# Kernel optimization log

Hardware: AMD Instinct MI355X
Metric: run time of the kernel (lower is better)

Reference implementation:

```python
import jax, jax.numpy as jnp
import numpy as np

N = 100000   # nodes
E = 1600000  # edges (avg degree 16)
G = 1024     # graphs in batch
F = 128      # node feature dim
H = 128      # hidden channels


def setup_inputs() -> dict:
    key = jax.random.key(0)
    ks = jax.random.split(key, 12)
    s = 1.0 / np.sqrt(H)
    x = jax.random.normal(ks[0], (N, F), dtype=jnp.float32)
    edge_index = jax.random.randint(ks[1], (2, E), 0, N, dtype=jnp.int32)
    batch = jnp.sort(jax.random.randint(ks[2], (N,), 0, G, dtype=jnp.int32))
    return {
        "x": x,
        "edge_index": edge_index,
        "batch": batch,
        "W1": jax.random.normal(ks[3], (F, H), dtype=jnp.float32) * s,
        "b1": jnp.zeros((H,), jnp.float32),
        "W2": jax.random.normal(ks[4], (H, H), dtype=jnp.float32) * s,
        "b2": jnp.zeros((H,), jnp.float32),
        "W3": jax.random.normal(ks[5], (H, H), dtype=jnp.float32) * s,
        "b3": jnp.zeros((H,), jnp.float32),
        "W4": jax.random.normal(ks[6], (H, H), dtype=jnp.float32) * s,
        "b4": jnp.zeros((H,), jnp.float32),
        "linW": jax.random.normal(ks[7], (H, 2), dtype=jnp.float32) * s,
        "linb": jnp.zeros((2,), jnp.float32),
    }


def _gcn_conv(h, W, b, src, dst, norm, n):
    # h' = D^{-1/2}(A+I)D^{-1/2} (h W) + b   (PyG GCNConv default)
    m = h @ W                              # [n, H]
    msg = m[src] * norm[:, None]           # [E+n, H] gather + scale
    out = jax.ops.segment_sum(msg, dst, num_segments=n)
    return out + b


def reference(x, edge_index, batch, W1, b1, W2, b2, W3, b3, W4, b4, linW, linb):
    n = x.shape[0]
    loops = jnp.arange(n, dtype=edge_index.dtype)
    src = jnp.concatenate([edge_index[0], loops])   # add self-loops
    dst = jnp.concatenate([edge_index[1], loops])
    deg = jax.ops.segment_sum(jnp.ones_like(dst, dtype=x.dtype), dst, num_segments=n)
    dinv = jax.lax.rsqrt(deg)                       # deg >= 1 due to self-loops
    norm = dinv[src] * dinv[dst]                    # [E+n]

    h = jax.nn.relu(_gcn_conv(x, W1, b1, src, dst, norm, n))
    h = jax.nn.relu(_gcn_conv(h, W2, b2, src, dst, norm, n))
    h = jax.nn.relu(_gcn_conv(h, W3, b3, src, dst, norm, n))
    h = jax.nn.relu(_gcn_conv(h, W4, b4, src, dst, norm, n))

    # global_mean_pool over `batch` segment ids
    counts = jax.ops.segment_sum(jnp.ones((n,), x.dtype), batch, num_segments=G)
    pooled = jax.ops.segment_sum(h, batch, num_segments=G) / jnp.maximum(counts, 1.0)[:, None]

    # dropout p=0.5 is identity in eval mode
    return pooled @ linW + linb
```

## Files before the change

### kernel.cpp

```cpp
#include <hip/hip_runtime.h>
#include <math.h>

#define NF 128
#define NU 64
#define NQ 32
#define TROWS 32
#define ARS 68
#define CRS 132
#define QS  16.0f
#define QIS 0.0625f

#define SRC_BITS 18
#define SRC_MASK ((1u << SRC_BITS) - 1u)
#define BCS 32
#define EPB 2048

typedef unsigned int  u32;
typedef unsigned short u16;
typedef u32 b4 __attribute__((ext_vector_type(2)));
typedef short bf16x8 __attribute__((ext_vector_type(8)));
typedef float f32x4 __attribute__((ext_vector_type(4)));
typedef float f32x2 __attribute__((ext_vector_type(2)));

__device__ inline u16 f2bf(float f) {
    u32 u = __float_as_uint(f);
    return (u16)((u + 0x7fffu + ((u >> 16) & 1u)) >> 16);
}
__device__ inline u32 pack2(float a, float b) {
    return (u32)f2bf(a) | ((u32)f2bf(b) << 16);
}
__device__ inline float bflo(u32 u) { return __uint_as_float(u << 16); }
__device__ inline float bfhi(u32 u) { return __uint_as_float(u & 0xffff0000u); }

__device__ inline u32 pack4(float a, float b, float c, float d) {
    u32 v = __builtin_amdgcn_cvt_pk_fp8_f32(a, b, 0, false);
    v = __builtin_amdgcn_cvt_pk_fp8_f32(c, d, v, true);
    return v;
}
__device__ inline void acc4(float4& a, u32 q) {
    f32x2 lo = __builtin_amdgcn_cvt_pk_f32_fp8(q, false);
    f32x2 hi = __builtin_amdgcn_cvt_pk_f32_fp8(q, true);
    a.x += lo[0]; a.y += lo[1]; a.z += hi[0]; a.w += hi[1];
}


__global__ __launch_bounds__(256) void k_bcnt(const int* __restrict__ ei,
                                              int* bcnt, int E, int bshift) {
    __shared__ int h[256];
    int t = threadIdx.x;
    h[t] = 0;
    __syncthreads();
    int base = blockIdx.x * EPB;
    #pragma unroll
    for (int k = 0; k < EPB / 256; ++k) {
        int e = base + k * 256 + t;
        if (e < E) atomicAdd(&h[ei[E + e] >> bshift], 1);
    }
    __syncthreads();
    if (h[t]) atomicAdd(&bcnt[t * BCS], h[t]);
}

__global__ __launch_bounds__(256) void k_bscan(const int* __restrict__ bcnt,
                                               int* bbase, int* bcur) {
    __shared__ int s[256];
    int t = threadIdx.x;
    int v = bcnt[t * BCS];
    s[t] = v;
    for (int d = 1; d < 256; d <<= 1) {
        __syncthreads();
        int a = (t >= d) ? s[t - d] : 0;
        __syncthreads();
        s[t] += a;
    }
    __syncthreads();
    bbase[t + 1] = s[t];
    bcur[t * BCS] = s[t] - v;
    if (t == 0) bbase[0] = 0;
}

__global__ __launch_bounds__(256) void k_bscat(const int* __restrict__ ei,
                                               int* bcur, u32* __restrict__ pairs,
                                               int E, int bshift) {
    __shared__ int h[256];
    __shared__ int rb[256];
    int t = threadIdx.x;
    h[t] = 0;
    __syncthreads();
    int base = blockIdx.x * EPB;
    #pragma unroll
    for (int k = 0; k < EPB / 256; ++k) {
        int e = base + k * 256 + t;
        if (e < E) atomicAdd(&h[ei[E + e] >> bshift], 1);
    }
    __syncthreads();
    int c = h[t];
    if (c) rb[t] = atomicAdd(&bcur[t * BCS], c);
    h[t] = 0;
    __syncthreads();
    #pragma unroll
    for (int k = 0; k < EPB / 256; ++k) {
        int e = base + k * 256 + t;
        if (e < E) {
            int d = ei[E + e];
            int b = d >> bshift;
            int p = rb[b] + atomicAdd(&h[b], 1);
            u32 rel = (u32)(d - (b << bshift));
            pairs[p] = (rel << SRC_BITS) | (u32)ei[e];
        }
    }
}

__global__ __launch_bounds__(512) void k_degscan(const u32* __restrict__ pairs,
        const int* __restrict__ bbase, float* __restrict__ dinv,
        int* __restrict__ offs, int* __restrict__ bsum, int n, int bshift) {
    extern __shared__ int sh[];
    int bsz = 1 << bshift;
    int* deg = sh;
    int* ss = sh + bsz;
    int b = blockIdx.x, b0 = b << bshift, t = threadIdx.x;
    for (int i = t; i < bsz; i += 512) deg[i] = 0;
    __syncthreads();
    int lo = bbase[b], hi = bbase[b + 1];
    for (int j = lo + t; j < hi; j += 512)
        atomicAdd(&deg[pairs[j] >> SRC_BITS], 1);
    __syncthreads();
    int C = bsz >> 9;
    int vloc[8];
    int tsum = 0;
    for (int c = 0; c < C; ++c) {
        int i = t * C + c;
        int node = b0 + i;
        int v = 0;
        if (node < n) {
            int real = deg[i] + 1;
            dinv[node] = 1.0f / sqrtf((float)real);
            v = (real + 3) & ~3;
        }
        vloc[c] = tsum;
        tsum += v;
    }
    ss[t] = tsum;
    for (int d = 1; d < 512; d <<= 1) {
        __syncthreads();
        int a = (t >= d) ? ss[t - d] : 0;
        __syncthreads();
        ss[t] += a;
    }
    __syncthreads();
    int tbase = ss[t] - tsum;
    for (int c = 0; c < C; ++c) {
        int node = b0 + t * C + c;
        if (node < n) offs[node] = tbase + vloc[c];
    }
    if (t == 511) bsum[b] = ss[511];
}

__global__ __launch_bounds__(256) void k_bktscan(int* bsum, int* offs,
                                                 int nbk, int n) {
    __shared__ int s[256];
    int t = threadIdx.x;
    int v = (t < nbk) ? bsum[t] : 0;
    s[t] = v;
    for (int d = 1; d < 256; d <<= 1) {
        __syncthreads();
        int a = (t >= d) ? s[t - d] : 0;
        __syncthreads();
        s[t] += a;
    }
    __syncthreads();
    if (t < nbk) bsum[t] = s[t] - v;
    if (t == 255) offs[n] = s[255];
}

__global__ __launch_bounds__(512) void k_csr(const u32* __restrict__ pairs,
        const int* __restrict__ bbase, const int* __restrict__ bsum,
        int* __restrict__ offs, int* __restrict__ srcS,
        int n, int nbk, int bshift) {
    extern __shared__ int sh[];
    int bsz = 1 << bshift;
    int* cur = sh;
    int* endv = sh + bsz;
    int b = blockIdx.x, b0 = b << bshift, t = threadIdx.x;
    int base = bsum[b];
    for (int i = t; i < bsz; i += 512) {
        int node = b0 + i;
        int o = 0;
        if (node < n) {
            o = offs[node] + base;
            offs[node] = o;
        }
        cur[i] = o;
    }
    __syncthreads();
    int offs_n = offs[n];
    for (int i = t; i < bsz; i += 512) {
        int node = b0 + i;
        int e;
        if (i < bsz - 1) e = (node + 1 < n) ? cur[i + 1] : offs_n;
        else             e = (b + 1 < nbk) ? bsum[b + 1] : offs_n;
        endv[i] = e;
    }
    __syncthreads();
    int lo = bbase[b], hi = bbase[b + 1];
    for (int j = lo + t; j < hi; j += 512) {
        u32 v = pairs[j];
        int p = atomicAdd(&cur[v >> SRC_BITS], 1);
        srcS[p] = (int)(v & SRC_MASK);
    }
    __syncthreads();
    for (int i = t; i < bsz; i += 512) {
        int node = b0 + i;
        if (node < n) {
            int c = cur[i];
            srcS[c] = node;
            int e = endv[i];
            for (int k = c + 1; k < e; ++k) srcS[k] = n;
        }
    }
}

__global__ __launch_bounds__(256) void k_pack(const float* __restrict__ x,
                       const float* __restrict__ dinv, u32* __restrict__ q,
                       const float* __restrict__ W0, const float* __restrict__ W1,
                       const float* __restrict__ W2, const float* __restrict__ W3,
                       u32* __restrict__ wt, int n) {
    int t = blockIdx.x * blockDim.x + threadIdx.x;
    int totalu4 = (n + 1) * (NQ / 4);
    if (t < totalu4) {
        int row = t >> 3;
        uint4 o = make_uint4(0, 0, 0, 0);
        if (row < n) {
            int cbase = (t & 7) << 4;
            const float* xr = x + (size_t)row * NF + cbase;
            float4 f0 = *(const float4*)(xr);
            float4 f1 = *(const float4*)(xr + 4);
            float4 f2 = *(const float4*)(xr + 8);
            float4 f3 = *(const float4*)(xr + 12);
            float d = dinv[row] * QS;
            o.x = pack4(f0.x * d, f0.y * d, f0.z * d, f0.w * d);
            o.y = pack4(f1.x * d, f1.y * d, f1.z * d, f1.w * d);
            o.z = pack4(f2.x * d, f2.y * d, f2.z * d, f2.w * d);
            o.w = pack4(f3.x * d, f3.y * d, f3.z * d, f3.w * d);
        }
        ((uint4*)q)[t] = o;
    }
    if (t < 4 * 2048) {
        int layer = t >> 11;
        int rem = t & 2047;
        int lane = rem & 63;
        int ks = (rem >> 6) & 3;
        int nt = rem >> 8;
        const float* W = layer == 0 ? W0 : layer == 1 ? W1 : layer == 2 ? W2 : W3;
        int nn = nt * 16 + (lane & 15);
        int k0 = ks * 32 + (lane >> 4) * 8;
        uint4 o;
        o.x = pack2(W[(k0 + 0) * NF + nn], W[(k0 + 1) * NF + nn]);
        o.y = pack2(W[(k0 + 2) * NF + nn], W[(k0 + 3) * NF + nn]);
        o.z = pack2(W[(k0 + 4) * NF + nn], W[(k0 + 5) * NF + nn]);
        o.w = pack2(W[(k0 + 6) * NF + nn], W[(k0 + 7) * NF + nn]);
        ((uint4*)wt)[t] = o;
    }
}

__global__ __launch_bounds__(256, 8) void k_fused(
        const u32* __restrict__ hin, const int* __restrict__ offs,
        const int* __restrict__ srcS, const float* __restrict__ dinv,
        const u32* __restrict__ wt, const float* __restrict__ bias,
        u32* __restrict__ out, int* tctr, int n, int ntiles, int last) {
    __shared__ __align__(16) u32 buf[TROWS * CRS];
    __shared__ int stile;
    float* Cs = (float*)buf;
    int tid = threadIdx.x;
    int grp = tid >> 5;
    int lane32 = tid & 31;
    int c4 = lane32 << 2;
    int cu = lane32 << 1;
    int cq = lane32;
    int wv = tid >> 6;
    int lane = tid & 63;
    int m0 = (wv & 1) * 16;
    int nh = wv >> 1;
    int mrow = lane & 15, quad = lane >> 4;

    float4 bv = *(const float4*)(bias + c4);

    for (;;) {
        if (tid == 0) stile = atomicAdd(tctr, 1);
        __syncthreads();
        int tile = stile;
        if (tile >= ntiles) break;
        int row0 = tile * TROWS;

        #pragma unroll
        for (int i = 0; i < 4; ++i) {
            int r = grp * 4 + i;
            int node = row0 + r;
            float4 acc = make_float4(0.f, 0.f, 0.f, 0.f);
            if (node < n) {
                int b = offs[node], e = offs[node + 1];
                int j = b;
                for (; j + 8 <= e; j += 8) {
                    int4 sa = *(const int4*)(srcS + j);
                    int4 sb = *(const int4*)(srcS + j + 4);
                    u32 q0 = hin[(size_t)sa.x * NQ + cq];
                    u32 q1 = hin[(size_t)sa.y * NQ + cq];
                    u32 q2 = hin[(size_t)sa.z * NQ + cq];
                    u32 q3 = hin[(size_t)sa.w * NQ + cq];
                    u32 q4 = hin[(size_t)sb.x * NQ + cq];
                    u32 q5 = hin[(size_t)sb.y * NQ + cq];
                    u32 q6 = hin[(size_t)sb.z * NQ + cq];
                    u32 q7 = hin[(size_t)sb.w * NQ + cq];
                    acc4(acc, q0); acc4(acc, q1); acc4(acc, q2); acc4(acc, q3);
                    acc4(acc, q4); acc4(acc, q5); acc4(acc, q6); acc4(acc, q7);
                }
                if (j < e) {
                    int4 sa = *(const int4*)(srcS + j);
                    u32 q0 = hin[(size_t)sa.x * NQ + cq];
                    u32 q1 = hin[(size_t)sa.y * NQ + cq];
                    u32 q2 = hin[(size_t)sa.z * NQ + cq];
                    u32 q3 = hin[(size_t)sa.w * NQ + cq];
                    acc4(acc, q0); acc4(acc, q1); acc4(acc, q2); acc4(acc, q3);
                }
                float dn = dinv[node];
                acc.x *= dn; acc.y *= dn; acc.z *= dn; acc.w *= dn;
            }
            b4 o; o.x = pack2(acc.x, acc.y); o.y = pack2(acc.z, acc.w);
            *(b4*)(buf + r * ARS + cu) = o;
        }
        __syncthreads();

        f32x4 a0 = {0.f, 0.f, 0.f, 0.f}, a1 = a0, a2 = a0, a3 = a0;
        #pragma unroll
        for (int ks = 0; ks < 4; ++ks) {
            bf16x8 a = *(const bf16x8*)(buf + (m0 + mrow) * ARS + ks * 16 + quad * 4);
            const u32* wb = wt + (((nh * 4) * 4 + ks) * 64 + lane) * 4;
            bf16x8 b0 = *(const bf16x8*)(wb);
            bf16x8 b1 = *(const bf16x8*)(wb + 1024);
            bf16x8 b2 = *(const bf16x8*)(wb + 2048);
            bf16x8 b3 = *(const bf16x8*)(wb + 3072);
            a0 = __builtin_amdgcn_mfma_f32_16x16x32_bf16(a, b0, a0, 0, 0, 0);
            a1 = __builtin_amdgcn_mfma_f32_16x16x32_bf16(a, b1, a1, 0, 0, 0);
            a2 = __builtin_amdgcn_mfma_f32_16x16x32_bf16(a, b2, a2, 0, 0, 0);
            a3 = __builtin_amdgcn_mfma_f32_16x16x32_bf16(a, b3, a3, 0, 0, 0);
        }
        __syncthreads();

        #pragma unroll
        for (int nt = 0; nt < 4; ++nt) {
            f32x4 av = nt == 0 ? a0 : nt == 1 ? a1 : nt == 2 ? a2 : a3;
            int col = (nh * 4 + nt) * 16 + mrow;
            #pragma unroll
            for (int rg = 0; rg < 4; ++rg)
                Cs[(m0 + quad * 4 + rg) * CRS + col] = av[rg];
        }
        __syncthreads();

        #pragma unroll
        for (int j = 0; j < 4; ++j) {
            int r = grp * 4 + j;
            int gr = row0 + r;
            if (gr <= n) {
                if (last) {
                    b4 o; o.x = 0u; o.y = 0u;
                    if (gr < n) {
                        float4 v = *(const float4*)(Cs + r * CRS + c4);
                        float ox = fmaxf(v.x * QIS + bv.x, 0.f);
                        float oy = fmaxf(v.y * QIS + bv.y, 0.f);
                        float oz = fmaxf(v.z * QIS + bv.z, 0.f);
                        float ow = fmaxf(v.w * QIS + bv.w, 0.f);
                        o.x = pack2(ox, oy);
                        o.y = pack2(oz, ow);
                    }
                    *(b4*)(out + (size_t)gr * NU + cu) = o;
                } else {
                    u32 o = 0u;
                    if (gr < n) {
                        float4 v = *(const float4*)(Cs + r * CRS + c4);
                        float sc = dinv[gr] * QS;
                        float ox = fmaxf(v.x * QIS + bv.x, 0.f) * sc;
                        float oy = fmaxf(v.y * QIS + bv.y, 0.f) * sc;
                        float oz = fmaxf(v.z * QIS + bv.z, 0.f) * sc;
                        float ow = fmaxf(v.w * QIS + bv.w, 0.f) * sc;
                        o = pack4(ox, oy, oz, ow);
                    }
                    out[(size_t)gr * NQ + cq] = o;
                }
            }
        }
        __syncthreads();
    }
}


__global__ __launch_bounds__(256) void k_poolfinal(const u32* __restrict__ h,
        const int* __restrict__ batch, const float* __restrict__ linW,
        const float* __restrict__ linb, float* __restrict__ outp, int N) {
    int g = blockIdx.x;
    int tid = threadIdx.x;
    __shared__ int sb[2];
    if (tid < 2) {
        int target = g + tid;
        int lo = 0, hi = N;
        while (lo < hi) {
            int mid = (lo + hi) >> 1;
            if (batch[mid] < target) lo = mid + 1; else hi = mid;
        }
        sb[tid] = lo;
    }
    __syncthreads();
    int b = sb[0], e = sb[1];

    int grp = tid >> 5, lane = tid & 31;
    int c4 = lane << 2, cu = lane << 1;
    float4 acc = make_float4(0.f, 0.f, 0.f, 0.f);
    for (int i = b + grp; i < e; i += 8) {
        b4 v = *(const b4*)(h + (size_t)i * NU + cu);
        acc.x += bflo(v.x); acc.y += bfhi(v.x);
        acc.z += bflo(v.y); acc.w += bfhi(v.y);
    }
    __shared__ float red[8][NF];
    *(float4*)(&red[grp][c4]) = acc;
    __syncthreads();

    float v0 = 0.f, v1 = 0.f;
    if (tid < NF) {
        float s = 0.f;
        #pragma unroll
        for (int gg = 0; gg < 8; ++gg) s += red[gg][tid];
        v0 = s * linW[tid * 2 + 0];
        v1 = s * linW[tid * 2 + 1];
    }
    #pragma unroll
    for (int d = 32; d > 0; d >>= 1) {
        v0 += __shfl_down(v0, d);
        v1 += __shfl_down(v1, d);
    }
    __shared__ float sv[8];
    if ((tid & 63) == 0) { sv[(tid >> 6) * 2] = v0; sv[(tid >> 6) * 2 + 1] = v1; }
    __syncthreads();
    if (tid == 0) {
        float inv = 1.0f / fmaxf((float)(e - b), 1.0f);
        outp[g * 2 + 0] = (sv[0] + sv[2]) * inv + linb[0];
        outp[g * 2 + 1] = (sv[1] + sv[3]) * inv + linb[1];
    }
}


extern "C" void kernel_launch(void* const* d_in, const int* in_sizes, int n_in,
                              void* d_out, int out_size, void* d_ws, size_t ws_size,
                              hipStream_t stream) {
    const float* x     = (const float*)d_in[0];
    const int*   ei    = (const int*)d_in[1];
    const int*   batch = (const int*)d_in[2];
    const float* Wl[4] = {(const float*)d_in[3], (const float*)d_in[5],
                          (const float*)d_in[7], (const float*)d_in[9]};
    const float* bl[4] = {(const float*)d_in[4], (const float*)d_in[6],
                          (const float*)d_in[8], (const float*)d_in[10]};
    const float* linW  = (const float*)d_in[11];
    const float* linb  = (const float*)d_in[12];
    float* out = (float*)d_out;

    const int N  = in_sizes[2];
    const int E  = in_sizes[1] / 2;
    const int G  = out_size / 2;

    int bshift = 9;
    while (((N + (1 << bshift) - 1) >> bshift) > 256) ++bshift;
    int nbk = (N + (1 << bshift) - 1) >> bshift;
    int bsz = 1 << bshift;

    char* p = (char*)d_ws;
    auto carve = [&](size_t bytes) -> char* {
        char* r = p;
        p += (bytes + 255) & ~(size_t)255;
        return r;
    };
    float* dinv   = (float*)carve((size_t)N * 4);
    int*   offs   = (int*)  carve((size_t)(N + 1) * 4);
    int*   bsum   = (int*)  carve(512 * 4);
    int*   bcnt   = (int*)  carve(256 * BCS * 4);
    int*   bbase  = (int*)  carve(257 * 4);
    int*   bcur   = (int*)  carve(256 * BCS * 4);
    int*   tctr   = (int*)  carve(4 * 4);
    u32*   wt     = (u32*)  carve(4 * 2048 * 16);
    int*   srcS   = (int*)  carve((size_t)(E + 4 * (size_t)N) * 4);
    u32*   bufA   = (u32*)  carve((size_t)(N + 1) * NU * 4);
    u32*   bufB   = (u32*)  carve((size_t)(N + 1) * NU * 4);
    u32*   pairs  = bufB;

    (void)hipMemsetAsync(bcnt, 0, 256 * BCS * 4, stream);
    (void)hipMemsetAsync(tctr, 0, 4 * 4, stream);

    int nblkE = (E + EPB - 1) / EPB;
    k_bcnt<<<nblkE, 256, 0, stream>>>(ei, bcnt, E, bshift);
    k_bscan<<<1, 256, 0, stream>>>(bcnt, bbase, bcur);
    k_bscat<<<nblkE, 256, 0, stream>>>(ei, bcur, pairs, E, bshift);
    k_degscan<<<nbk, 512, (bsz + 512) * 4, stream>>>(pairs, bbase, dinv, offs,
                                                     bsum, N, bshift);
    k_bktscan<<<1, 256, 0, stream>>>(bsum, offs, nbk, N);
    k_csr<<<nbk, 512, 2 * bsz * 4, stream>>>(pairs, bbase, bsum, offs, srcS,
                                             N, nbk, bshift);

    int totalu4 = (N + 1) * (NQ / 4);
    int packT = totalu4 > 8192 ? totalu4 : 8192;
    k_pack<<<(packT + 255) / 256, 256, 0, stream>>>(x, dinv, bufA,
                                                    Wl[0], Wl[1], Wl[2], Wl[3], wt, N);

    int ntiles = (N + 1 + TROWS - 1) / TROWS;
    int ngrid = ntiles < 2048 ? ntiles : 2048;
    const u32* hin = bufA;
    u32* hout = bufB;
    for (int l = 0; l < 4; ++l) {
        k_fused<<<ngrid, 256, 0, stream>>>(hin, offs, srcS, dinv, wt + l * 8192,
                                           bl[l], hout, tctr + l, N, ntiles, l == 3);
        hin = hout;
        hout = (hout == bufA) ? bufB : bufA;
    }

    k_poolfinal<<<G, 256, 0, stream>>>(hin, batch, linW, linb, out, N);
}
```

Measured before the change: 547.8 us.

## Interleave two nodes' neighbor gathers with prefetched indices and nontemporal loads

The aggregation loop now processes two destination rows at once, walking both CSR neighbor lists in lockstep four edges at a time. It prefetches the next index vectors with nontemporal loads while the current gathers are in flight, which raises memory-level parallelism and hides index-load latency. Shorter lists are padded with a sentinel zero row, which relies on the CSR padding to multiples of four. The x reads in the pack kernel use nontemporal loads, and the two memsets are merged into one spanning bcnt through tctr. Uneven degrees within a pair waste gather slots on sentinel reads.

```diff
diff --git a/kernel.cpp b/kernel.cpp
--- a/kernel.cpp
+++ b/kernel.cpp
@@ -21,6 +21,7 @@
 typedef short bf16x8 __attribute__((ext_vector_type(8)));
 typedef float f32x4 __attribute__((ext_vector_type(4)));
 typedef float f32x2 __attribute__((ext_vector_type(2)));
+typedef int   int4v __attribute__((ext_vector_type(4)));
 
 __device__ inline u16 f2bf(float f) {
     u32 u = __float_as_uint(f);
@@ -41,6 +42,9 @@
     f32x2 lo = __builtin_amdgcn_cvt_pk_f32_fp8(q, false);
     f32x2 hi = __builtin_amdgcn_cvt_pk_f32_fp8(q, true);
     a.x += lo[0]; a.y += lo[1]; a.z += hi[0]; a.w += hi[1];
+}
+__device__ inline int4v nt4(const int* p) {
+    return __builtin_nontemporal_load((const int4v*)p);
 }
 
 
@@ -232,10 +236,10 @@
         if (row < n) {
             int cbase = (t & 7) << 4;
             const float* xr = x + (size_t)row * NF + cbase;
-            float4 f0 = *(const float4*)(xr);
-            float4 f1 = *(const float4*)(xr + 4);
-            float4 f2 = *(const float4*)(xr + 8);
-            float4 f3 = *(const float4*)(xr + 12);
+            f32x4 f0 = __builtin_nontemporal_load((const f32x4*)(xr));
+            f32x4 f1 = __builtin_nontemporal_load((const f32x4*)(xr + 4));
+            f32x4 f2 = __builtin_nontemporal_load((const f32x4*)(xr + 8));
+            f32x4 f3 = __builtin_nontemporal_load((const f32x4*)(xr + 12));
             float d = dinv[row] * QS;
             o.x = pack4(f0.x * d, f0.y * d, f0.z * d, f0.w * d);
             o.y = pack4(f1.x * d, f1.y * d, f1.z * d, f1.w * d);
@@ -292,40 +296,44 @@
         int row0 = tile * TROWS;
 
         #pragma unroll
-        for (int i = 0; i < 4; ++i) {
-            int r = grp * 4 + i;
-            int node = row0 + r;
-            float4 acc = make_float4(0.f, 0.f, 0.f, 0.f);
-            if (node < n) {
-                int b = offs[node], e = offs[node + 1];
-                int j = b;
-                for (; j + 8 <= e; j += 8) {
-                    int4 sa = *(const int4*)(srcS + j);
-                    int4 sb = *(const int4*)(srcS + j + 4);
-                    u32 q0 = hin[(size_t)sa.x * NQ + cq];
-                    u32 q1 = hin[(size_t)sa.y * NQ + cq];
-                    u32 q2 = hin[(size_t)sa.z * NQ + cq];
-                    u32 q3 = hin[(size_t)sa.w * NQ + cq];
-                    u32 q4 = hin[(size_t)sb.x * NQ + cq];
-                    u32 q5 = hin[(size_t)sb.y * NQ + cq];
-                    u32 q6 = hin[(size_t)sb.z * NQ + cq];
-                    u32 q7 = hin[(size_t)sb.w * NQ + cq];
-                    acc4(acc, q0); acc4(acc, q1); acc4(acc, q2); acc4(acc, q3);
-                    acc4(acc, q4); acc4(acc, q5); acc4(acc, q6); acc4(acc, q7);
-                }
-                if (j < e) {
-                    int4 sa = *(const int4*)(srcS + j);
-                    u32 q0 = hin[(size_t)sa.x * NQ + cq];
-                    u32 q1 = hin[(size_t)sa.y * NQ + cq];
-                    u32 q2 = hin[(size_t)sa.z * NQ + cq];
-                    u32 q3 = hin[(size_t)sa.w * NQ + cq];
-                    acc4(acc, q0); acc4(acc, q1); acc4(acc, q2); acc4(acc, q3);
-                }
-                float dn = dinv[node];
-                acc.x *= dn; acc.y *= dn; acc.z *= dn; acc.w *= dn;
+        for (int pr = 0; pr < 2; ++pr) {
+            int rA = grp * 4 + pr * 2;
+            int nodeA = row0 + rA;
+            int nodeB = nodeA + 1;
+            int bA = 0, eA = 0, bB = 0, eB = 0;
+            float dA = 0.f, dB = 0.f;
+            if (nodeA < n) { bA = offs[nodeA]; eA = offs[nodeA + 1]; dA = dinv[nodeA]; }
+            if (nodeB < n) { bB = offs[nodeB]; eB = offs[nodeB + 1]; dB = dinv[nodeB]; }
+            float4 accA = make_float4(0.f, 0.f, 0.f, 0.f);
+            float4 accB = make_float4(0.f, 0.f, 0.f, 0.f);
+            int lenA = eA - bA, lenB = eB - bB;
+            int lmax = lenA > lenB ? lenA : lenB;
+            int jA = bA, jB = bB;
+            int4v sent = {n, n, n, n};
+            int4v sA = (lenA > 0) ? nt4(srcS + jA) : sent;
+            int4v sB = (lenB > 0) ? nt4(srcS + jB) : sent;
+            for (int k = 0; k < lmax; k += 4) {
+                u32 qa0 = hin[(size_t)sA.x * NQ + cq];
+                u32 qa1 = hin[(size_t)sA.y * NQ + cq];
+                u32 qa2 = hin[(size_t)sA.z * NQ + cq];
+                u32 qa3 = hin[(size_t)sA.w * NQ + cq];
+                u32 qb0 = hin[(size_t)sB.x * NQ + cq];
+                u32 qb1 = hin[(size_t)sB.y * NQ + cq];
+                u32 qb2 = hin[(size_t)sB.z * NQ + cq];
+                u32 qb3 = hin[(size_t)sB.w * NQ + cq];
+                jA += 4; jB += 4;
+                int4v nA = (jA < eA) ? nt4(srcS + jA) : sent;
+                int4v nB = (jB < eB) ? nt4(srcS + jB) : sent;
+                acc4(accA, qa0); acc4(accA, qa1); acc4(accA, qa2); acc4(accA, qa3);
+                acc4(accB, qb0); acc4(accB, qb1); acc4(accB, qb2); acc4(accB, qb3);
+                sA = nA; sB = nB;
             }
-            b4 o; o.x = pack2(acc.x, acc.y); o.y = pack2(acc.z, acc.w);
-            *(b4*)(buf + r * ARS + cu) = o;
+            accA.x *= dA; accA.y *= dA; accA.z *= dA; accA.w *= dA;
+            accB.x *= dB; accB.y *= dB; accB.z *= dB; accB.w *= dB;
+            b4 oA; oA.x = pack2(accA.x, accA.y); oA.y = pack2(accA.z, accA.w);
+            b4 oB; oB.x = pack2(accB.x, accB.y); oB.y = pack2(accB.z, accB.w);
+            *(b4*)(buf + rA * ARS + cu) = oA;
+            *(b4*)(buf + (rA + 1) * ARS + cu) = oB;
         }
         __syncthreads();
 
@@ -488,8 +496,8 @@
     u32*   bufB   = (u32*)  carve((size_t)(N + 1) * NU * 4);
     u32*   pairs  = bufB;
 
-    (void)hipMemsetAsync(bcnt, 0, 256 * BCS * 4, stream);
-    (void)hipMemsetAsync(tctr, 0, 4 * 4, stream);
+    size_t zbytes = (char*)(tctr + 4) - (char*)bcnt;
+    (void)hipMemsetAsync(bcnt, 0, zbytes, stream);
 
     int nblkE = (E + EPB - 1) / EPB;
     k_bcnt<<<nblkE, 256, 0, stream>>>(ei, bcnt, E, bshift);
```

Measured after the change: 606.6 us. 1.11x slower.

## Scatter edges into fixed-capacity buckets and fold scans to drop preprocessing kernels

Applied to the files above, without the earlier changes.

Edges are now scattered into per-bucket regions of fixed capacity, so the separate bucket-count and bucket-scan passes go away. The bucket-sum scan moves into k_csr, where each block redundantly computes the prefix. Two memsets become one, and the x loads in k_pack become nontemporal. This cuts three kernel launches and one full pass over the edge array. In exchange it relies on a capacity bound (1.25x the average plus slack) that could overflow on skewed destination distributions.

```diff
diff --git a/kernel.cpp b/kernel.cpp
--- a/kernel.cpp
+++ b/kernel.cpp
@@ -44,9 +44,11 @@
 }
 
 
-__global__ __launch_bounds__(256) void k_bcnt(const int* __restrict__ ei,
-                                              int* bcnt, int E, int bshift) {
+__global__ __launch_bounds__(256) void k_bscat(const int* __restrict__ ei,
+                                               int* bcur, u32* __restrict__ pairs,
+                                               int E, int bshift, int cap) {
     __shared__ int h[256];
+    __shared__ int rb[256];
     int t = threadIdx.x;
     h[t] = 0;
     __syncthreads();
@@ -57,44 +59,8 @@
         if (e < E) atomicAdd(&h[ei[E + e] >> bshift], 1);
     }
     __syncthreads();
-    if (h[t]) atomicAdd(&bcnt[t * BCS], h[t]);
-}
-
-__global__ __launch_bounds__(256) void k_bscan(const int* __restrict__ bcnt,
-                                               int* bbase, int* bcur) {
-    __shared__ int s[256];
-    int t = threadIdx.x;
-    int v = bcnt[t * BCS];
-    s[t] = v;
-    for (int d = 1; d < 256; d <<= 1) {
-        __syncthreads();
-        int a = (t >= d) ? s[t - d] : 0;
-        __syncthreads();
-        s[t] += a;
-    }
-    __syncthreads();
-    bbase[t + 1] = s[t];
-    bcur[t * BCS] = s[t] - v;
-    if (t == 0) bbase[0] = 0;
-}
-
-__global__ __launch_bounds__(256) void k_bscat(const int* __restrict__ ei,
-                                               int* bcur, u32* __restrict__ pairs,
-                                               int E, int bshift) {
-    __shared__ int h[256];
-    __shared__ int rb[256];
-    int t = threadIdx.x;
-    h[t] = 0;
-    __syncthreads();
-    int base = blockIdx.x * EPB;
-    #pragma unroll
-    for (int k = 0; k < EPB / 256; ++k) {
-        int e = base + k * 256 + t;
-        if (e < E) atomicAdd(&h[ei[E + e] >> bshift], 1);
-    }
-    __syncthreads();
     int c = h[t];
-    if (c) rb[t] = atomicAdd(&bcur[t * BCS], c);
+    if (c) rb[t] = t * cap + atomicAdd(&bcur[t * BCS], c);
     h[t] = 0;
     __syncthreads();
     #pragma unroll
@@ -111,8 +77,9 @@
 }
 
 __global__ __launch_bounds__(512) void k_degscan(const u32* __restrict__ pairs,
-        const int* __restrict__ bbase, float* __restrict__ dinv,
-        int* __restrict__ offs, int* __restrict__ bsum, int n, int bshift) {
+        const int* __restrict__ bcur, float* __restrict__ dinv,
+        int* __restrict__ offs, int* __restrict__ bsum,
+        int n, int bshift, int cap) {
     extern __shared__ int sh[];
     int bsz = 1 << bshift;
     int* deg = sh;
@@ -120,7 +87,7 @@
     int b = blockIdx.x, b0 = b << bshift, t = threadIdx.x;
     for (int i = t; i < bsz; i += 512) deg[i] = 0;
     __syncthreads();
-    int lo = bbase[b], hi = bbase[b + 1];
+    int lo = b * cap, hi = lo + bcur[b * BCS];
     for (int j = lo + t; j < hi; j += 512)
         atomicAdd(&deg[pairs[j] >> SRC_BITS], 1);
     __syncthreads();
@@ -155,33 +122,32 @@
     if (t == 511) bsum[b] = ss[511];
 }
 
-__global__ __launch_bounds__(256) void k_bktscan(int* bsum, int* offs,
-                                                 int nbk, int n) {
-    __shared__ int s[256];
-    int t = threadIdx.x;
-    int v = (t < nbk) ? bsum[t] : 0;
-    s[t] = v;
-    for (int d = 1; d < 256; d <<= 1) {
-        __syncthreads();
-        int a = (t >= d) ? s[t - d] : 0;
-        __syncthreads();
-        s[t] += a;
-    }
-    __syncthreads();
-    if (t < nbk) bsum[t] = s[t] - v;
-    if (t == 255) offs[n] = s[255];
-}
-
 __global__ __launch_bounds__(512) void k_csr(const u32* __restrict__ pairs,
-        const int* __restrict__ bbase, const int* __restrict__ bsum,
+        const int* __restrict__ bcur, const int* __restrict__ bsum,
         int* __restrict__ offs, int* __restrict__ srcS,
-        int n, int nbk, int bshift) {
+        int n, int nbk, int bshift, int cap) {
     extern __shared__ int sh[];
+    __shared__ int ss[512];
     int bsz = 1 << bshift;
     int* cur = sh;
     int* endv = sh + bsz;
     int b = blockIdx.x, b0 = b << bshift, t = threadIdx.x;
-    int base = bsum[b];
+
+    int v = (t < nbk) ? bsum[t] : 0;
+    ss[t] = v;
+    for (int d = 1; d < 512; d <<= 1) {
+        __syncthreads();
+        int a = (t >= d) ? ss[t - d] : 0;
+        __syncthreads();
+        ss[t] += a;
+    }
+    __syncthreads();
+    int bsumb = bsum[b];
+    int base = ss[b] - bsumb;
+    int nextbase = ss[b];
+    int total = ss[511];
+    if (b == nbk - 1 && t == 0) offs[n] = total;
+
     for (int i = t; i < bsz; i += 512) {
         int node = b0 + i;
         int o = 0;
@@ -192,20 +158,20 @@
         cur[i] = o;
     }
     __syncthreads();
-    int offs_n = offs[n];
     for (int i = t; i < bsz; i += 512) {
         int node = b0 + i;
         int e;
-        if (i < bsz - 1) e = (node + 1 < n) ? cur[i + 1] : offs_n;
-        else             e = (b + 1 < nbk) ? bsum[b + 1] : offs_n;
+        if (node + 1 >= n)       e = total;
+        else if (i < bsz - 1)    e = cur[i + 1];
+        else                     e = nextbase;
         endv[i] = e;
     }
     __syncthreads();
-    int lo = bbase[b], hi = bbase[b + 1];
+    int lo = b * cap, hi = lo + bcur[b * BCS];
     for (int j = lo + t; j < hi; j += 512) {
-        u32 v = pairs[j];
-        int p = atomicAdd(&cur[v >> SRC_BITS], 1);
-        srcS[p] = (int)(v & SRC_MASK);
+        u32 vv = pairs[j];
+        int p = atomicAdd(&cur[vv >> SRC_BITS], 1);
+        srcS[p] = (int)(vv & SRC_MASK);
     }
     __syncthreads();
     for (int i = t; i < bsz; i += 512) {
@@ -232,10 +198,10 @@
         if (row < n) {
             int cbase = (t & 7) << 4;
             const float* xr = x + (size_t)row * NF + cbase;
-            float4 f0 = *(const float4*)(xr);
-            float4 f1 = *(const float4*)(xr + 4);
-            float4 f2 = *(const float4*)(xr + 8);
-            float4 f3 = *(const float4*)(xr + 12);
+            f32x4 f0 = __builtin_nontemporal_load((const f32x4*)(xr));
+            f32x4 f1 = __builtin_nontemporal_load((const f32x4*)(xr + 4));
+            f32x4 f2 = __builtin_nontemporal_load((const f32x4*)(xr + 8));
+            f32x4 f3 = __builtin_nontemporal_load((const f32x4*)(xr + 12));
             float d = dinv[row] * QS;
             o.x = pack4(f0.x * d, f0.y * d, f0.z * d, f0.w * d);
             o.y = pack4(f1.x * d, f1.y * d, f1.z * d, f1.w * d);
@@ -468,6 +434,7 @@
     while (((N + (1 << bshift) - 1) >> bshift) > 256) ++bshift;
     int nbk = (N + (1 << bshift) - 1) >> bshift;
     int bsz = 1 << bshift;
+    int cap = ((E / nbk) * 5 / 4 + 1024 + 255) & ~255;
 
     char* p = (char*)d_ws;
     auto carve = [&](size_t bytes) -> char* {
@@ -478,8 +445,6 @@
     float* dinv   = (float*)carve((size_t)N * 4);
     int*   offs   = (int*)  carve((size_t)(N + 1) * 4);
     int*   bsum   = (int*)  carve(512 * 4);
-    int*   bcnt   = (int*)  carve(256 * BCS * 4);
-    int*   bbase  = (int*)  carve(257 * 4);
     int*   bcur   = (int*)  carve(256 * BCS * 4);
     int*   tctr   = (int*)  carve(4 * 4);
     u32*   wt     = (u32*)  carve(4 * 2048 * 16);
@@ -488,18 +453,15 @@
     u32*   bufB   = (u32*)  carve((size_t)(N + 1) * NU * 4);
     u32*   pairs  = bufB;
 
-    (void)hipMemsetAsync(bcnt, 0, 256 * BCS * 4, stream);
-    (void)hipMemsetAsync(tctr, 0, 4 * 4, stream);
+    size_t zbytes = (char*)(tctr + 4) - (char*)bcur;
+    (void)hipMemsetAsync(bcur, 0, zbytes, stream);
 
     int nblkE = (E + EPB - 1) / EPB;
-    k_bcnt<<<nblkE, 256, 0, stream>>>(ei, bcnt, E, bshift);
-    k_bscan<<<1, 256, 0, stream>>>(bcnt, bbase, bcur);
-    k_bscat<<<nblkE, 256, 0, stream>>>(ei, bcur, pairs, E, bshift);
-    k_degscan<<<nbk, 512, (bsz + 512) * 4, stream>>>(pairs, bbase, dinv, offs,
-                                                     bsum, N, bshift);
-    k_bktscan<<<1, 256, 0, stream>>>(bsum, offs, nbk, N);
-    k_csr<<<nbk, 512, 2 * bsz * 4, stream>>>(pairs, bbase, bsum, offs, srcS,
-                                             N, nbk, bshift);
+    k_bscat<<<nblkE, 256, 0, stream>>>(ei, bcur, pairs, E, bshift, cap);
+    k_degscan<<<nbk, 512, (bsz + 512) * 4, stream>>>(pairs, bcur, dinv, offs,
+                                                     bsum, N, bshift, cap);
+    k_csr<<<nbk, 512, 2 * bsz * 4, stream>>>(pairs, bcur, bsum, offs, srcS,
+                                             N, nbk, bshift, cap);
 
     int totalu4 = (N + 1) * (NQ / 4);
     int packT = totalu4 > 8192 ? totalu4 : 8192;
```

Result: no change. 538.0 us (-1.8%).
